# Performance work log

Hardware: AMD Instinct MI355X
Metric: run time of the kernel (lower is better)

Reference implementation:

```python
import jax, jax.numpy as jnp
import numpy as np

N_TAGS = 30
START_ID = 25
END_ID = 26
HID = 768
H = HID // 2  # per-direction hidden = 384
NEG = -10000.0


def _lstm_dir(x, w_ih, w_hh, b_ih, b_hh, reverse):
    # x: [B,T,D]; w_ih: [4H,D]; w_hh: [4H,H]; biases: [4H]
    B = x.shape[0]
    h = w_hh.shape[1]
    pre = jnp.einsum('btd,gd->btg', x, w_ih) + b_ih + b_hh  # [B,T,4H]

    def step(carry, p_t):
        hprev, cprev = carry
        g = p_t + hprev @ w_hh.T
        i, f, gg, o = jnp.split(g, 4, axis=-1)  # torch gate order i,f,g,o
        i = jax.nn.sigmoid(i)
        f = jax.nn.sigmoid(f)
        gg = jnp.tanh(gg)
        o = jax.nn.sigmoid(o)
        c = f * cprev + i * gg
        hn = o * jnp.tanh(c)
        return (hn, c), hn

    init = (jnp.zeros((B, h), x.dtype), jnp.zeros((B, h), x.dtype))
    _, hs = jax.lax.scan(step, init, pre.swapaxes(0, 1), reverse=reverse)
    return hs.swapaxes(0, 1)  # [B,T,H]


def _bilstm(x, p):
    h1 = jnp.concatenate([
        _lstm_dir(x, p['w_ih_l0f'], p['w_hh_l0f'], p['b_ih_l0f'], p['b_hh_l0f'], False),
        _lstm_dir(x, p['w_ih_l0b'], p['w_hh_l0b'], p['b_ih_l0b'], p['b_hh_l0b'], True),
    ], axis=-1)  # [B,T,768]
    h2 = jnp.concatenate([
        _lstm_dir(h1, p['w_ih_l1f'], p['w_hh_l1f'], p['b_ih_l1f'], p['b_hh_l1f'], False),
        _lstm_dir(h1, p['w_ih_l1b'], p['w_hh_l1b'], p['b_ih_l1b'], p['b_hh_l1b'], True),
    ], axis=-1)
    return h2


def _viterbi(feats, transitions):
    # feats: [B,T,K]. Faithful to torch: log_delta starts at -10000 everywhere
    # (the original never sets the start tag in _viterbi_decode) and feats[:,0]
    # is never added.
    B, T, K = feats.shape
    init = jnp.full((B, K), NEG, feats.dtype)

    def step(ld, feat_t):
        m = transitions[None, :, :] + ld[:, None, :]  # [B,K_next,K_prev]
        best = jnp.max(m, axis=-1)
        idx = jnp.argmax(m, axis=-1).astype(jnp.int32)
        return best + feat_t, idx

    ld_final, psis = jax.lax.scan(step, init, feats[:, 1:].swapaxes(0, 1))  # psis: [T-1,B,K]
    score = jnp.max(ld_final, axis=-1)  # [B]
    last = jnp.argmax(ld_final, axis=-1).astype(jnp.int32)  # [B]

    def back(tag, psi_t):
        prev = jnp.take_along_axis(psi_t, tag[:, None], axis=1)[:, 0]
        return prev, prev

    _, rev = jax.lax.scan(back, last, psis, reverse=True)  # rev[t] = path[t], t=0..T-2
    path = jnp.concatenate([rev, last[None, :]], axis=0).swapaxes(0, 1)  # [B,T]
    return score, path


def setup_inputs() -> dict:
    key = jax.random.key(0)
    ks = jax.random.split(key, 24)
    B, T, D = 64, 512, 768
    s = 0.03  # small init scale for LSTM/FC params
    inp = {'embeds': jax.random.normal(ks[0], (B, T, D), jnp.float32)}
    trans = jax.random.normal(ks[1], (N_TAGS, N_TAGS), jnp.float32)
    trans = trans.at[START_ID, :].set(NEG).at[:, END_ID].set(NEG)
    inp['transitions'] = trans
    inp['fc_w'] = jax.random.normal(ks[2], (N_TAGS, HID), jnp.float32) * s
    inp['fc_b'] = jnp.zeros((N_TAGS,), jnp.float32)
    i = 3
    for layer, din in (('l0', 768), ('l1', 768)):
        for d in ('f', 'b'):
            inp[f'w_ih_{layer}{d}'] = jax.random.normal(ks[i], (4 * H, din), jnp.float32) * s; i += 1
            inp[f'w_hh_{layer}{d}'] = jax.random.normal(ks[i], (4 * H, H), jnp.float32) * s; i += 1
            inp[f'b_ih_{layer}{d}'] = jnp.zeros((4 * H,), jnp.float32)
            inp[f'b_hh_{layer}{d}'] = jnp.zeros((4 * H,), jnp.float32)
    return inp


def reference(embeds, transitions, fc_w, fc_b,
              w_ih_l0f, w_hh_l0f, b_ih_l0f, b_hh_l0f,
              w_ih_l0b, w_hh_l0b, b_ih_l0b, b_hh_l0b,
              w_ih_l1f, w_hh_l1f, b_ih_l1f, b_hh_l1f,
              w_ih_l1b, w_hh_l1b, b_ih_l1b, b_hh_l1b):
    p = dict(w_ih_l0f=w_ih_l0f, w_hh_l0f=w_hh_l0f, b_ih_l0f=b_ih_l0f, b_hh_l0f=b_hh_l0f,
             w_ih_l0b=w_ih_l0b, w_hh_l0b=w_hh_l0b, b_ih_l0b=b_ih_l0b, b_hh_l0b=b_hh_l0b,
             w_ih_l1f=w_ih_l1f, w_hh_l1f=w_hh_l1f, b_ih_l1f=b_ih_l1f, b_hh_l1f=b_hh_l1f,
             w_ih_l1b=w_ih_l1b, w_hh_l1b=w_hh_l1b, b_ih_l1b=b_ih_l1b, b_hh_l1b=b_hh_l1b)
    enc = _bilstm(embeds, p)                      # [B,T,768]
    feats = enc @ fc_w.T + fc_b                   # [B,T,n_tags]
    score, path = _viterbi(feats, transitions)
    return score, path
```

## Files before the change

### kernel.cpp

```cpp
#include <hip/hip_runtime.h>
#include <math.h>


#define B_    64
#define T_    512
#define D_    768
#define H_    384
#define G4    1536
#define NTAGS 30
#define TC    64
#define NCH   (T_ / TC)

typedef float f32x4 __attribute__((ext_vector_type(4)));

__device__ __forceinline__ float sigm(float x) { return 1.f / (1.f + expf(-x)); }

__global__ __launch_bounds__(256)
void sgemm_pre(const float* __restrict__ A, int t0f, int t0b,
               const float* __restrict__ Wf, const float* __restrict__ Wb,
               const float* __restrict__ b1f, const float* __restrict__ b2f,
               const float* __restrict__ b1b, const float* __restrict__ b2b,
               float* __restrict__ outF, float* __restrict__ outB) {
  const int z = blockIdx.z;
  const int t0 = z ? t0b : t0f;
  const float* __restrict__ W  = z ? Wb  : Wf;
  const float* __restrict__ b1 = z ? b1b : b1f;
  const float* __restrict__ b2 = z ? b2b : b2f;
  float* __restrict__ Cc = z ? outB : outF;

  __shared__ float As[16][128];
  __shared__ float Bs[16][128];
  const int tid = threadIdx.x;
  const int bm = blockIdx.y * 128;
  const int bn = blockIdx.x * 128;
  const int tx = tid & 15;
  const int ty = tid >> 4;

  float acc[8][8];
  #pragma unroll
  for (int i = 0; i < 8; ++i)
    #pragma unroll
    for (int j = 0; j < 8; ++j) acc[i][j] = 0.f;

  for (int k0 = 0; k0 < D_; k0 += 16) {
    #pragma unroll
    for (int s = tid; s < 512; s += 256) {
      int r = s >> 2, k4 = (s & 3) * 4;
      int rl = bm + r;
      const float* arow = A + ((size_t)(rl >> 6) * T_ + t0 + (rl & 63)) * D_;
      float4 va = *(const float4*)(arow + k0 + k4);
      As[k4 + 0][r] = va.x; As[k4 + 1][r] = va.y;
      As[k4 + 2][r] = va.z; As[k4 + 3][r] = va.w;
      float4 vb = *(const float4*)(W + (size_t)(bn + r) * D_ + k0 + k4);
      Bs[k4 + 0][r] = vb.x; Bs[k4 + 1][r] = vb.y;
      Bs[k4 + 2][r] = vb.z; Bs[k4 + 3][r] = vb.w;
    }
    __syncthreads();
    #pragma unroll
    for (int k = 0; k < 16; ++k) {
      float a[8], bv[8];
      *(float4*)(a)      = *(const float4*)&As[k][ty * 4];
      *(float4*)(a + 4)  = *(const float4*)&As[k][64 + ty * 4];
      *(float4*)(bv)     = *(const float4*)&Bs[k][tx * 4];
      *(float4*)(bv + 4) = *(const float4*)&Bs[k][64 + tx * 4];
      #pragma unroll
      for (int i = 0; i < 8; ++i)
        #pragma unroll
        for (int j = 0; j < 8; ++j)
          acc[i][j] += a[i] * bv[j];
    }
    __syncthreads();
  }

  float4 b1l = *(const float4*)(b1 + bn + tx * 4);
  float4 b2l = *(const float4*)(b2 + bn + tx * 4);
  float4 b1h = *(const float4*)(b1 + bn + 64 + tx * 4);
  float4 b2h = *(const float4*)(b2 + bn + 64 + tx * 4);
  float4 bl = {b1l.x + b2l.x, b1l.y + b2l.y, b1l.z + b2l.z, b1l.w + b2l.w};
  float4 bh = {b1h.x + b2h.x, b1h.y + b2h.y, b1h.z + b2h.z, b1h.w + b2h.w};

  #pragma unroll
  for (int i = 0; i < 8; ++i) {
    int r = (i < 4) ? (ty * 4 + i) : (64 + ty * 4 + (i - 4));
    size_t row = (size_t)(bm + r);
    float4 lo = {acc[i][0] + bl.x, acc[i][1] + bl.y, acc[i][2] + bl.z, acc[i][3] + bl.w};
    float4 hi = {acc[i][4] + bh.x, acc[i][5] + bh.y, acc[i][6] + bh.z, acc[i][7] + bh.w};
    *(float4*)(Cc + row * G4 + bn + tx * 4)      = lo;
    *(float4*)(Cc + row * G4 + bn + 64 + tx * 4) = hi;
  }
}

template<int LAYER>
__global__ __launch_bounds__(256, 1)
void lstm_chunk(const float* __restrict__ preF, const float* __restrict__ preB,
                const float* __restrict__ whhF, const float* __restrict__ whhB,
                float* __restrict__ hbuf, float* __restrict__ h2cF, float* __restrict__ h2cB,
                float* __restrict__ h_g, float* __restrict__ c_g,
                unsigned* __restrict__ flags, int chunk, unsigned seqBase) {
  const int bid    = blockIdx.x;
  const int stream = bid & 31;
  const int wg     = bid >> 5;
  const int dir    = stream & 1;
  const int bg     = stream >> 1;
  const int tid    = threadIdx.x;
  const int g      = tid >> 6;
  const int lane   = tid & 63;
  const int ks     = lane & 15;
  const int ug     = lane >> 4;

  const float* __restrict__ pre = dir ? preB : preF;
  const float* __restrict__ whh = dir ? whhB : whhF;

  __shared__ float h_lds[4 * 448];
  __shared__ float gLDS[4 * 192];
  __shared__ float lds_pad[18432];

  if (flags[300] == 0xDEADBEEFu) lds_pad[tid] = 1.f;

  f32x4 W[12][6];
  {
    const float* wsrc = whh + ((size_t)(g * H_ + wg * 48 + ug * 12)) * H_ + ks * 24;
    #pragma unroll
    for (int r = 0; r < 12; ++r)
      #pragma unroll
      for (int jj = 0; jj < 6; ++jj)
        W[r][jj] = *(const f32x4*)(wsrc + (size_t)r * H_ + jj * 4);
  }

  const int own_u = tid % 48;
  const int own_b = tid / 48;
  float c_own = 0.f;
  if (chunk > 0 && tid < 192)
    c_own = c_g[(size_t)(stream * 8 + wg) * 192 + tid];

  float* hg0 = h_g + (size_t)stream * 1536;
  float* hg1 = h_g + (size_t)(32 + stream) * 1536;

  if (chunk == 0) {
    for (int i = tid; i < 4 * 448; i += 256) h_lds[i] = 0.f;
  } else {
    {
      int f = tid;
      int b = f / 96, k4 = (f % 96) * 4;
      float4 v = *(const float4*)(hg0 + b * 384 + k4);
      *(float4*)&h_lds[b * 448 + (k4 / 24) * 28 + (k4 % 24)] = v;
    }
    if (tid < 128) {
      int f = tid + 256;
      int b = f / 96, k4 = (f % 96) * 4;
      float4 v = *(const float4*)(hg0 + b * 384 + k4);
      *(float4*)&h_lds[b * 448 + (k4 / 24) * 28 + (k4 % 24)] = v;
    }
  }
  __syncthreads();

  const int ucol = wg * 48;

  for (int s = 0; s < TC; ++s) {
    const int t  = dir ? (T_ - 1 - chunk * TC - s) : (chunk * TC + s);
    const int lt = dir ? (TC - 1 - s) : s;
    const unsigned seq = seqBase + (unsigned)s + 1u;
    const int par = (s + 1) & 1;

    float pv0, pv1, pv2, pv3;
    if (tid < 192) {
      const size_t pbase = ((size_t)(bg * 4 + own_b) * TC + lt) * G4 + ucol + own_u;
      pv0 = pre[pbase];           pv1 = pre[pbase + H_];
      pv2 = pre[pbase + 2 * H_];  pv3 = pre[pbase + 3 * H_];
    }

    float acc[12][4];
    #pragma unroll
    for (int r = 0; r < 12; ++r)
      #pragma unroll
      for (int b = 0; b < 4; ++b) acc[r][b] = 0.f;

    const int hcol = ks * 28;
    #pragma unroll
    for (int kq = 0; kq < 6; ++kq) {
      f32x4 h4[4];
      #pragma unroll
      for (int b = 0; b < 4; ++b)
        h4[b] = *(const f32x4*)&h_lds[b * 448 + hcol + kq * 4];
      #pragma unroll
      for (int r = 0; r < 12; ++r) {
        f32x4 w4 = W[r][kq];
        #pragma unroll
        for (int b = 0; b < 4; ++b)
          acc[r][b] += w4.x * h4[b].x + w4.y * h4[b].y
                     + w4.z * h4[b].z + w4.w * h4[b].w;
      }
    }

    const bool up8 = (ks & 8) != 0;
    const bool up4 = (ks & 4) != 0;
    const int bsel = ((ks >> 3) & 1) * 2 + ((ks >> 2) & 1);
    #pragma unroll
    for (int r = 0; r < 12; ++r) {
      float s0 = up8 ? acc[r][0] : acc[r][2];
      float s1 = up8 ? acc[r][1] : acc[r][3];
      float r0 = __shfl_xor(s0, 8, 64);
      float r1 = __shfl_xor(s1, 8, 64);
      float a0 = (up8 ? acc[r][2] : acc[r][0]) + r0;
      float a1 = (up8 ? acc[r][3] : acc[r][1]) + r1;
      float ss = up4 ? a0 : a1;
      float rr = __shfl_xor(ss, 4, 64);
      float v  = (up4 ? a1 : a0) + rr;
      v += __shfl_xor(v, 2, 64);
      v += __shfl_xor(v, 1, 64);
      if ((ks & 3) == 0)
        gLDS[g * 192 + (ug * 12 + r) * 4 + bsel] = v;
    }
    __syncthreads();

    if (tid < 192) {
      float gi = sigm(gLDS[0 * 192 + own_u * 4 + own_b] + pv0);
      float gf = sigm(gLDS[1 * 192 + own_u * 4 + own_b] + pv1);
      float gg = tanhf(gLDS[2 * 192 + own_u * 4 + own_b] + pv2);
      float go = sigm(gLDS[3 * 192 + own_u * 4 + own_b] + pv3);
      c_own = gf * c_own + gi * gg;
      float h_new = go * tanhf(c_own);

      float* hg_w = par ? hg1 : hg0;
      asm volatile("global_store_dword %0, %1, off sc0 sc1"
                   :: "v"(hg_w + own_b * 384 + ucol + own_u), "v"(h_new) : "memory");

      const int bglob = bg * 4 + own_b;
      if (LAYER == 0)
        hbuf[((size_t)bglob * T_ + t) * 768 + dir * H_ + ucol + own_u] = h_new;
      else
        (dir ? h2cB : h2cF)[((size_t)bglob * TC + lt) * H_ + ucol + own_u] = h_new;
    }
    asm volatile("s_waitcnt vmcnt(0)" ::: "memory");
    __syncthreads();
    if (tid == 0)
      asm volatile("global_store_dword %0, %1, off sc0 sc1"
                   :: "v"(&flags[stream * 8 + wg]), "v"(seq) : "memory");
    if (s == TC - 1) break;

    if (tid < 8) {
      const unsigned* fp = &flags[stream * 8 + tid];
      unsigned v;
      while (true) {
        asm volatile("global_load_dword %0, %1, off sc0 sc1\n\ts_waitcnt vmcnt(0)"
                     : "=v"(v) : "v"(fp) : "memory");
        if (v >= seq) break;
        __builtin_amdgcn_s_sleep(1);
      }
    }
    __syncthreads();

    {
      const float* src = par ? hg1 : hg0;
      f32x4 tmp0, tmp1;
      {
        int f = tid;
        int b = f / 96, k4 = (f % 96) * 4;
        asm volatile("global_load_dwordx4 %0, %1, off sc0 sc1"
                     : "=v"(tmp0) : "v"(src + b * 384 + k4) : "memory");
      }
      if (tid < 128) {
        int f = tid + 256;
        int b = f / 96, k4 = (f % 96) * 4;
        asm volatile("global_load_dwordx4 %0, %1, off sc0 sc1"
                     : "=v"(tmp1) : "v"(src + b * 384 + k4) : "memory");
      }
      asm volatile("s_waitcnt vmcnt(0)" ::: "memory");
      __builtin_amdgcn_sched_barrier(0);
      {
        int f = tid;
        int b = f / 96, k4 = (f % 96) * 4;
        *(f32x4*)&h_lds[b * 448 + (k4 / 24) * 28 + (k4 % 24)] = tmp0;
      }
      if (tid < 128) {
        int f = tid + 256;
        int b = f / 96, k4 = (f % 96) * 4;
        *(f32x4*)&h_lds[b * 448 + (k4 / 24) * 28 + (k4 % 24)] = tmp1;
      }
    }
    __syncthreads();
  }

  if (tid < 192)
    c_g[(size_t)(stream * 8 + wg) * 192 + tid] = c_own;
}

__global__ __launch_bounds__(256)
void feats_init(const float* __restrict__ fc_b, float* __restrict__ feats) {
  const int n = threadIdx.x & 31;
  const size_t row = (size_t)blockIdx.x * 8 + (threadIdx.x >> 5);
  if (n >= NTAGS) return;
  feats[row * NTAGS + n] = fc_b[n];
}

__global__ __launch_bounds__(256)
void fc_half(const float* __restrict__ h2cF, const float* __restrict__ h2cB,
             const float* __restrict__ fc_w,
             float* __restrict__ feats, int t0f, int t0b) {
  const int z = blockIdx.z;
  const float* __restrict__ h2c = z ? h2cB : h2cF;
  const int coff = z ? H_ : 0;
  const int t0   = z ? t0b : t0f;

  const int tid = threadIdx.x;
  const int n  = tid & 31;
  const int rl = tid >> 5;
  const int row_loc = blockIdx.x * 8 + rl;
  if (n >= NTAGS) return;
  const int b  = row_loc >> 6;
  const int lt = row_loc & 63;
  const float* x = h2c + (size_t)row_loc * H_;
  const float* w = fc_w + (size_t)n * D_ + coff;
  float acc = 0.f;
  #pragma unroll 8
  for (int k = 0; k < H_; k += 4) {
    float4 xv = *(const float4*)(x + k);
    float4 wv = *(const float4*)(w + k);
    acc += xv.x * wv.x + xv.y * wv.y + xv.z * wv.z + xv.w * wv.w;
  }
  feats[((size_t)b * T_ + t0 + lt) * NTAGS + n] += acc;
}

__global__ __launch_bounds__(64)
void viterbi_kernel(const float* __restrict__ feats,
                    const float* __restrict__ trans,
                    float* __restrict__ score_out, float* __restrict__ path_out) {
  const int b = blockIdx.x;
  const int lane = threadIdx.x;
  __shared__ float trs[NTAGS * NTAGS];
  __shared__ float ld[32];
  __shared__ unsigned char psi[T_ - 1][NTAGS];

  for (int i = lane; i < NTAGS * NTAGS; i += 64) trs[i] = trans[i];
  if (lane < NTAGS) ld[lane] = -10000.0f;
  __syncthreads();

  for (int t = 1; t < T_; ++t) {
    float best = -INFINITY; int arg = 0;
    if (lane < NTAGS) {
      #pragma unroll
      for (int p = 0; p < NTAGS; ++p) {
        float v = trs[lane * NTAGS + p] + ld[p];
        if (v > best) { best = v; arg = p; }
      }
    }
    __syncthreads();
    if (lane < NTAGS) {
      ld[lane] = best + feats[((size_t)b * T_ + t) * NTAGS + lane];
      psi[t - 1][lane] = (unsigned char)arg;
    }
    __syncthreads();
  }

  if (lane == 0) {
    float best = ld[0]; int last = 0;
    #pragma unroll
    for (int p = 1; p < NTAGS; ++p)
      if (ld[p] > best) { best = ld[p]; last = p; }
    score_out[b] = best;
    int tag = last;
    path_out[(size_t)b * T_ + (T_ - 1)] = (float)tag;
    for (int t = T_ - 2; t >= 0; --t) {
      tag = psi[t][tag];
      path_out[(size_t)b * T_ + t] = (float)tag;
    }
  }
}

extern "C" void kernel_launch(void* const* d_in, const int* in_sizes, int n_in,
                              void* d_out, int out_size, void* d_ws, size_t ws_size,
                              hipStream_t stream) {
  const float* embeds = (const float*)d_in[0];
  const float* trans  = (const float*)d_in[1];
  const float* fc_w   = (const float*)d_in[2];
  const float* fc_b   = (const float*)d_in[3];
  const float* w_ih[2][2] = {{(const float*)d_in[4],  (const float*)d_in[8]},
                             {(const float*)d_in[12], (const float*)d_in[16]}};
  const float* w_hh[2][2] = {{(const float*)d_in[5],  (const float*)d_in[9]},
                             {(const float*)d_in[13], (const float*)d_in[17]}};
  const float* b_ih[2][2] = {{(const float*)d_in[6],  (const float*)d_in[10]},
                             {(const float*)d_in[14], (const float*)d_in[18]}};
  const float* b_hh[2][2] = {{(const float*)d_in[7],  (const float*)d_in[11]},
                             {(const float*)d_in[15], (const float*)d_in[19]}};

  const size_t HB   = (size_t)B_ * T_ * 768;
  const size_t PRE  = (size_t)B_ * TC * G4;
  const size_t H2C  = (size_t)B_ * TC * H_;
  const size_t FT   = (size_t)B_ * T_ * NTAGS;
  const size_t HG   = (size_t)2 * 32 * 1536;
  const size_t CG   = (size_t)32 * 8 * 192;

  float* ws     = (float*)d_ws;
  float* hbuf   = ws;
  float* preF   = hbuf + HB;
  float* preB   = preF + PRE;
  float* h2cF   = preB + PRE;
  float* h2cB   = h2cF + H2C;
  float* feats  = h2cB + H2C;
  float* h_g    = feats + FT;
  float* c_g    = h_g + HG;
  unsigned* flags = (unsigned*)(c_g + CG);

  hipMemsetAsync(flags, 0, 512 * sizeof(unsigned), stream);
  feats_init<<<(B_ * T_) / 8, 256, 0, stream>>>(fc_b, feats);

  dim3 gg(G4 / 128, (B_ * TC) / 128, 2);

  for (int c = 0; c < NCH; ++c) {
    const int t0f = c * TC;
    const int t0b = T_ - (c + 1) * TC;
    sgemm_pre<<<gg, 256, 0, stream>>>(embeds, t0f, t0b, w_ih[0][0], w_ih[0][1],
                                      b_ih[0][0], b_hh[0][0], b_ih[0][1], b_hh[0][1],
                                      preF, preB);
    lstm_chunk<0><<<256, 256, 0, stream>>>(preF, preB, w_hh[0][0], w_hh[0][1],
                                           hbuf, nullptr, nullptr, h_g, c_g,
                                           flags, c, (unsigned)(c * TC));
  }

  for (int c = 0; c < NCH; ++c) {
    const int t0f = c * TC;
    const int t0b = T_ - (c + 1) * TC;
    sgemm_pre<<<gg, 256, 0, stream>>>(hbuf, t0f, t0b, w_ih[1][0], w_ih[1][1],
                                      b_ih[1][0], b_hh[1][0], b_ih[1][1], b_hh[1][1],
                                      preF, preB);
    lstm_chunk<1><<<256, 256, 0, stream>>>(preF, preB, w_hh[1][0], w_hh[1][1],
                                           nullptr, h2cF, h2cB, h_g, c_g,
                                           flags, c, (unsigned)(T_ + c * TC));
    dim3 gf((B_ * TC) / 8, 1, 2);
    fc_half<<<gf, 256, 0, stream>>>(h2cF, h2cB, fc_w, feats, t0f, t0b);
  }

  float* score = (float*)d_out;
  float* path  = score + B_;
  viterbi_kernel<<<B_, 64, 0, stream>>>(feats, trans, score, path);
}
```

Before: 11.48 ms.

## Replace flag barriers with tagged h-value pairs and double chunk length

Each hidden value is now stored together with a step tag as a float pair, so consumers spin directly on the data until every tag matches. This removes the per-step vmcnt wait, the block barrier, the separate flag store and the flag polling. The chunk length grows from 64 to 128 steps, which halves the number of sgemm/lstm/fc launches at the cost of larger pre-activation buffers. The pair stores double the traffic through the exchange buffer, and correctness depends on step tags being exactly representable as floats and never colliding with stale values.

```diff
diff --git a/kernel.cpp b/kernel.cpp
--- a/kernel.cpp
+++ b/kernel.cpp
@@ -8,10 +8,11 @@
 #define H_    384
 #define G4    1536
 #define NTAGS 30
-#define TC    64
+#define TC    128
 #define NCH   (T_ / TC)
 
 typedef float f32x4 __attribute__((ext_vector_type(4)));
+typedef float f32x2 __attribute__((ext_vector_type(2)));
 
 __device__ __forceinline__ float sigm(float x) { return 1.f / (1.f + expf(-x)); }
 
@@ -47,7 +48,7 @@
     for (int s = tid; s < 512; s += 256) {
       int r = s >> 2, k4 = (s & 3) * 4;
       int rl = bm + r;
-      const float* arow = A + ((size_t)(rl >> 6) * T_ + t0 + (rl & 63)) * D_;
+      const float* arow = A + ((size_t)(rl / TC) * T_ + t0 + (rl % TC)) * D_;
       float4 va = *(const float4*)(arow + k0 + k4);
       As[k4 + 0][r] = va.x; As[k4 + 1][r] = va.y;
       As[k4 + 2][r] = va.z; As[k4 + 3][r] = va.w;
@@ -95,8 +96,8 @@
 void lstm_chunk(const float* __restrict__ preF, const float* __restrict__ preB,
                 const float* __restrict__ whhF, const float* __restrict__ whhB,
                 float* __restrict__ hbuf, float* __restrict__ h2cF, float* __restrict__ h2cB,
-                float* __restrict__ h_g, float* __restrict__ c_g,
-                unsigned* __restrict__ flags, int chunk, unsigned seqBase) {
+                float* __restrict__ hpairs, float* __restrict__ c_g,
+                int chunk, unsigned seqBase) {
   const int bid    = blockIdx.x;
   const int stream = bid & 31;
   const int wg     = bid >> 5;
@@ -115,7 +116,7 @@
   __shared__ float gLDS[4 * 192];
   __shared__ float lds_pad[18432];
 
-  if (flags[300] == 0xDEADBEEFu) lds_pad[tid] = 1.f;
+  if (__float_as_uint(c_g[0]) == 0xDEADBEEFu) lds_pad[tid] = 1.f;
 
   f32x4 W[12][6];
   {
@@ -133,24 +134,38 @@
   if (chunk > 0 && tid < 192)
     c_own = c_g[(size_t)(stream * 8 + wg) * 192 + tid];
 
-  float* hg0 = h_g + (size_t)stream * 1536;
-  float* hg1 = h_g + (size_t)(32 + stream) * 1536;
+  float* hp0 = hpairs + (size_t)stream * 3072;
+  float* hp1 = hpairs + (size_t)(32 + stream) * 3072;
+
+  int ldsoff[3];
+  #pragma unroll
+  for (int i = 0; i < 3; ++i) {
+    int f  = tid + i * 256;
+    int b  = f / 192;
+    int u0 = 2 * (f % 192);
+    ldsoff[i] = b * 448 + (u0 / 24) * 28 + (u0 % 24);
+  }
 
   if (chunk == 0) {
     for (int i = tid; i < 4 * 448; i += 256) h_lds[i] = 0.f;
   } else {
-    {
-      int f = tid;
-      int b = f / 96, k4 = (f % 96) * 4;
-      float4 v = *(const float4*)(hg0 + b * 384 + k4);
-      *(float4*)&h_lds[b * 448 + (k4 / 24) * 28 + (k4 % 24)] = v;
-    }
-    if (tid < 128) {
-      int f = tid + 256;
-      int b = f / 96, k4 = (f % 96) * 4;
-      float4 v = *(const float4*)(hg0 + b * 384 + k4);
-      *(float4*)&h_lds[b * 448 + (k4 / 24) * 28 + (k4 % 24)] = v;
-    }
+    const float ftag = (float)(int)seqBase;
+    f32x4 v[3];
+    bool done = false;
+    while (!done) {
+      #pragma unroll
+      for (int i = 0; i < 3; ++i)
+        asm volatile("global_load_dwordx4 %0, %1, off sc0 sc1"
+                     : "=v"(v[i]) : "v"(hp0 + (size_t)(tid + i * 256) * 4) : "memory");
+      asm volatile("s_waitcnt vmcnt(0)" ::: "memory");
+      done = true;
+      #pragma unroll
+      for (int i = 0; i < 3; ++i) done = done && (v[i].y == ftag) && (v[i].w == ftag);
+      if (!done) __builtin_amdgcn_s_sleep(1);
+    }
+    #pragma unroll
+    for (int i = 0; i < 3; ++i)
+      *(f32x2*)&h_lds[ldsoff[i]] = f32x2{v[i].x, v[i].z};
   }
   __syncthreads();
 
@@ -159,8 +174,8 @@
   for (int s = 0; s < TC; ++s) {
     const int t  = dir ? (T_ - 1 - chunk * TC - s) : (chunk * TC + s);
     const int lt = dir ? (TC - 1 - s) : s;
-    const unsigned seq = seqBase + (unsigned)s + 1u;
-    const int par = (s + 1) & 1;
+    const float ftag = (float)(int)(seqBase + (unsigned)s + 1u);
+    float* hp_w = ((s + 1) & 1) ? hp1 : hp0;
 
     float pv0, pv1, pv2, pv3;
     if (tid < 192) {
@@ -221,9 +236,10 @@
       c_own = gf * c_own + gi * gg;
       float h_new = go * tanhf(c_own);
 
-      float* hg_w = par ? hg1 : hg0;
-      asm volatile("global_store_dword %0, %1, off sc0 sc1"
-                   :: "v"(hg_w + own_b * 384 + ucol + own_u), "v"(h_new) : "memory");
+      f32x2 pv = {h_new, ftag};
+      asm volatile("global_store_dwordx2 %0, %1, off sc0 sc1"
+                   :: "v"(hp_w + (size_t)(own_b * 384 + ucol + own_u) * 2), "v"(pv)
+                   : "memory");
 
       const int bglob = bg * 4 + own_b;
       if (LAYER == 0)
@@ -231,52 +247,25 @@
       else
         (dir ? h2cB : h2cF)[((size_t)bglob * TC + lt) * H_ + ucol + own_u] = h_new;
     }
-    asm volatile("s_waitcnt vmcnt(0)" ::: "memory");
-    __syncthreads();
-    if (tid == 0)
-      asm volatile("global_store_dword %0, %1, off sc0 sc1"
-                   :: "v"(&flags[stream * 8 + wg]), "v"(seq) : "memory");
     if (s == TC - 1) break;
 
-    if (tid < 8) {
-      const unsigned* fp = &flags[stream * 8 + tid];
-      unsigned v;
-      while (true) {
-        asm volatile("global_load_dword %0, %1, off sc0 sc1\n\ts_waitcnt vmcnt(0)"
-                     : "=v"(v) : "v"(fp) : "memory");
-        if (v >= seq) break;
-        __builtin_amdgcn_s_sleep(1);
+    {
+      f32x4 v[3];
+      bool done = false;
+      while (!done) {
+        #pragma unroll
+        for (int i = 0; i < 3; ++i)
+          asm volatile("global_load_dwordx4 %0, %1, off sc0 sc1"
+                       : "=v"(v[i]) : "v"(hp_w + (size_t)(tid + i * 256) * 4) : "memory");
+        asm volatile("s_waitcnt vmcnt(0)" ::: "memory");
+        done = true;
+        #pragma unroll
+        for (int i = 0; i < 3; ++i) done = done && (v[i].y == ftag) && (v[i].w == ftag);
+        if (!done) __builtin_amdgcn_s_sleep(1);
       }
-    }
-    __syncthreads();
-
-    {
-      const float* src = par ? hg1 : hg0;
-      f32x4 tmp0, tmp1;
-      {
-        int f = tid;
-        int b = f / 96, k4 = (f % 96) * 4;
-        asm volatile("global_load_dwordx4 %0, %1, off sc0 sc1"
-                     : "=v"(tmp0) : "v"(src + b * 384 + k4) : "memory");
-      }
-      if (tid < 128) {
-        int f = tid + 256;
-        int b = f / 96, k4 = (f % 96) * 4;
-        asm volatile("global_load_dwordx4 %0, %1, off sc0 sc1"
-                     : "=v"(tmp1) : "v"(src + b * 384 + k4) : "memory");
-      }
-      asm volatile("s_waitcnt vmcnt(0)" ::: "memory");
-      __builtin_amdgcn_sched_barrier(0);
-      {
-        int f = tid;
-        int b = f / 96, k4 = (f % 96) * 4;
-        *(f32x4*)&h_lds[b * 448 + (k4 / 24) * 28 + (k4 % 24)] = tmp0;
-      }
-      if (tid < 128) {
-        int f = tid + 256;
-        int b = f / 96, k4 = (f % 96) * 4;
-        *(f32x4*)&h_lds[b * 448 + (k4 / 24) * 28 + (k4 % 24)] = tmp1;
-      }
+      #pragma unroll
+      for (int i = 0; i < 3; ++i)
+        *(f32x2*)&h_lds[ldsoff[i]] = f32x2{v[i].x, v[i].z};
     }
     __syncthreads();
   }
@@ -307,8 +296,8 @@
   const int rl = tid >> 5;
   const int row_loc = blockIdx.x * 8 + rl;
   if (n >= NTAGS) return;
-  const int b  = row_loc >> 6;
-  const int lt = row_loc & 63;
+  const int b  = row_loc / TC;
+  const int lt = row_loc % TC;
   const float* x = h2c + (size_t)row_loc * H_;
   const float* w = fc_w + (size_t)n * D_ + coff;
   float acc = 0.f;
@@ -387,7 +376,7 @@
   const size_t PRE  = (size_t)B_ * TC * G4;
   const size_t H2C  = (size_t)B_ * TC * H_;
   const size_t FT   = (size_t)B_ * T_ * NTAGS;
-  const size_t HG   = (size_t)2 * 32 * 1536;
+  const size_t HP   = (size_t)2 * 32 * 3072;
   const size_t CG   = (size_t)32 * 8 * 192;
 
   float* ws     = (float*)d_ws;
@@ -397,11 +386,9 @@
   float* h2cF   = preB + PRE;
   float* h2cB   = h2cF + H2C;
   float* feats  = h2cB + H2C;
-  float* h_g    = feats + FT;
-  float* c_g    = h_g + HG;
-  unsigned* flags = (unsigned*)(c_g + CG);
-
-  hipMemsetAsync(flags, 0, 512 * sizeof(unsigned), stream);
+  float* hpairs = feats + FT;
+  float* c_g    = hpairs + HP;
+
   feats_init<<<(B_ * T_) / 8, 256, 0, stream>>>(fc_b, feats);
 
   dim3 gg(G4 / 128, (B_ * TC) / 128, 2);
@@ -413,8 +400,8 @@
                                       b_ih[0][0], b_hh[0][0], b_ih[0][1], b_hh[0][1],
                                       preF, preB);
     lstm_chunk<0><<<256, 256, 0, stream>>>(preF, preB, w_hh[0][0], w_hh[0][1],
-                                           hbuf, nullptr, nullptr, h_g, c_g,
-                                           flags, c, (unsigned)(c * TC));
+                                           hbuf, nullptr, nullptr, hpairs, c_g,
+                                           c, (unsigned)(c * TC));
   }
 
   for (int c = 0; c < NCH; ++c) {
@@ -424,8 +411,8 @@
                                       b_ih[1][0], b_hh[1][0], b_ih[1][1], b_hh[1][1],
                                       preF, preB);
     lstm_chunk<1><<<256, 256, 0, stream>>>(preF, preB, w_hh[1][0], w_hh[1][1],
-                                           nullptr, h2cF, h2cB, h_g, c_g,
-                                           flags, c, (unsigned)(T_ + c * TC));
+                                           nullptr, h2cF, h2cB, hpairs, c_g,
+                                           c, (unsigned)(T_ + c * TC));
     dim3 gf((B_ * TC) / 8, 1, 2);
     fc_half<<<gf, 256, 0, stream>>>(h2cF, h2cB, fc_w, feats, t0f, t0b);
   }
```

New measurement: 11.18 ms. -2.6%, faster.
